# Kernel optimization log

Measured on AMD Instinct MI355X. Metric: run time of the kernel, lower is better.

## Reference

```python
import jax, jax.numpy as jnp
import numpy as np

N_IN = 100_000
N_OUT = 800_000
K = 27          # 3x3x3 kernel offsets
C_IN = 32
C_OUT = 64


def setup_inputs() -> dict:
    key = jax.random.key(0)
    k1, k2, k3, k4, k5, k6 = jax.random.split(key, 6)
    feats = jax.random.normal(k1, (N_IN, C_IN), dtype=jnp.float32)
    weight = jax.random.normal(k2, (K, C_IN, C_OUT), dtype=jnp.float32) * (1.0 / np.sqrt(C_IN * K))
    bias = jax.random.normal(k3, (C_OUT,), dtype=jnp.float32) * 0.01
    # bwd is the inverse sort permutation cached by the paired downsampling conv
    bwd = jax.random.permutation(k4, N_IN).astype(jnp.int64)
    # rulebook: per kernel offset, (input row, output row) pairs
    in_idx = jax.random.randint(k5, (K, N_IN), 0, N_IN, dtype=jnp.int64)
    out_idx = jax.random.randint(k6, (K, N_IN), 0, N_OUT, dtype=jnp.int64)
    return {"feats": feats, "weight": weight, "bias": bias,
            "bwd": bwd, "in_idx": in_idx, "out_idx": out_idx, "n_out": N_OUT}


def reference(feats, weight, bias, bwd, in_idx, out_idx, n_out):
    # 1) recover original feature order (the x.feats[bwd] gather)
    f = feats[bwd]                                   # [N_in, C_in]
    # 2) rulebook gather-GEMM-scatter
    gathered = f[in_idx]                             # [K, P, C_in]
    contrib = jnp.einsum('kpc,kcd->kpd', gathered, weight)  # [K, P, C_out]
    out = jnp.zeros((n_out, C_OUT), dtype=feats.dtype)
    out = out.at[out_idx].add(contrib)               # scatter-add over rulebook
    out = out + bias
    return out
```

## Files before the change

### kernel.cpp

```cpp
#include <hip/hip_runtime.h>

#define C_IN  32
#define C_OUT 64
#define KK    27

using frag_ab = __attribute__((ext_vector_type(8))) short;
using frag_cd = __attribute__((ext_vector_type(4))) float;
using u32x4   = __attribute__((ext_vector_type(4))) unsigned int;

static __device__ inline unsigned short f2bf(float f) {
    unsigned u = __float_as_uint(f);
    return (unsigned short)((u + 0x7fffu + ((u >> 16) & 1u)) >> 16);
}
static __device__ inline unsigned pack2(float a, float b) {
    return (unsigned)f2bf(a) | ((unsigned)f2bf(b) << 16);
}
static __device__ inline float bflo(unsigned u) { return __uint_as_float(u << 16); }
static __device__ inline float bfhi(unsigned u) { return __uint_as_float(u & 0xffff0000u); }

__global__ __launch_bounds__(256) void sic_init_bias(float4* __restrict__ out4,
                                                     const float4* __restrict__ bias4,
                                                     int total4) {
    int idx = blockIdx.x * 256 + threadIdx.x, stride = gridDim.x * 256;
    for (int i = idx; i < total4; i += stride) out4[i] = bias4[i & 15];
}

__global__ __launch_bounds__(256) void sic_scatter(
    const float* __restrict__ feats, const float* __restrict__ weight,
    const int* __restrict__ bwd, const int* __restrict__ in_idx,
    const int* __restrict__ out_idx, float* __restrict__ out, int n_in)
{
    const int k = blockIdx.y, lane = threadIdx.x & 63, wid = threadIdx.x >> 6;
    float w[C_IN];
    const float* wk = weight + k * (C_IN * C_OUT);
#pragma unroll
    for (int i = 0; i < C_IN; ++i) w[i] = wk[i * C_OUT + lane];
    const int waves_total = gridDim.x * 4;
    const long long base = (long long)k * n_in;
    for (int p = blockIdx.x * 4 + wid; p < n_in; p += waves_total) {
        int src = __builtin_amdgcn_readfirstlane(in_idx[base + p]);
        int dst = __builtin_amdgcn_readfirstlane(out_idx[base + p]);
        int row = __builtin_amdgcn_readfirstlane(bwd[src]);
        const float* f = feats + (long long)row * C_IN;
        float acc = 0.0f;
#pragma unroll
        for (int i = 0; i < C_IN; ++i) acc = fmaf(f[i], w[i], acc);
        atomicAdd(out + (long long)dst * C_OUT + lane, acc);
    }
}

__global__ __launch_bounds__(512) void sic_zero(int* __restrict__ p, int n) {
    int i = blockIdx.x * 512 + threadIdx.x, stride = gridDim.x * 512;
    for (; i < n; i += stride) p[i] = 0;
}

__global__ __launch_bounds__(256) void sic_fconv(const float* __restrict__ feats,
                                                 short* __restrict__ featsbf, int n_in) {
    int t = blockIdx.x * 256 + threadIdx.x;
    if (t >= (n_in + 1) * 4) return;
    int row = t >> 2, c8 = (t & 3) * 8;
    uint4 v = {0u, 0u, 0u, 0u};
    if (row < n_in) {
        const float* fp = feats + (size_t)row * C_IN + c8;
        float4 f0 = ((const float4*)fp)[0];
        float4 f1 = ((const float4*)fp)[1];
        v.x = pack2(f0.x, f0.y);
        v.y = pack2(f0.z, f0.w);
        v.z = pack2(f1.x, f1.y);
        v.w = pack2(f1.z, f1.w);
    }
    ((uint4*)featsbf)[t] = v;
}

__global__ __launch_bounds__(256) void sic_wconv(const float* __restrict__ weight,
                                                 short* __restrict__ wfrag) {
    int t = blockIdx.x * 256 + threadIdx.x;
    if (t >= KK * 4 * 64) return;
    int l = t & 63, nb = (t >> 6) & 3, k = t >> 8;
    int g = l >> 4, cl = l & 15;
    const float* wp = weight + (size_t)k * (C_IN * C_OUT) + nb * 16 + cl;
    float r[8];
#pragma unroll
    for (int j = 0; j < 8; ++j) r[j] = wp[(size_t)(g * 8 + j) * C_OUT];
    uint4 v = {pack2(r[0], r[1]), pack2(r[2], r[3]), pack2(r[4], r[5]), pack2(r[6], r[7])};
    ((uint4*)wfrag)[t] = v;
}

__global__ __launch_bounds__(256) void sic_hist3(const int* __restrict__ out_idx_seg,
                                                 int* __restrict__ count,
                                                 int* __restrict__ ord, int pseg) {
    int i = blockIdx.x * 256 + threadIdx.x;
    if (i < pseg) {
        ord[i] = atomicAdd(&count[out_idx_seg[i]], 1);
    }
}

__global__ __launch_bounds__(512) void sic_scan_chunk(const int* __restrict__ in,
                                                      int* __restrict__ outExcl,
                                                      int* __restrict__ sums, int n) {
    __shared__ int sm[512];
    int tid = threadIdx.x, g = blockIdx.x * 512 + tid;
    int e = (g < n) ? in[g] : 0;
    sm[tid] = e;
    __syncthreads();
    for (int off = 1; off < 512; off <<= 1) {
        int t = (tid >= off) ? sm[tid - off] : 0;
        __syncthreads();
        sm[tid] += t;
        __syncthreads();
    }
    if (g < n) outExcl[g] = sm[tid] - e;
    if (tid == 511) sums[blockIdx.x] = sm[511];
}

__global__ __launch_bounds__(512) void sic_scan_small(int* __restrict__ buf, int n) {
    __shared__ int sm[512];
    int tid = threadIdx.x;
    int e = (tid < n) ? buf[tid] : 0;
    sm[tid] = e;
    __syncthreads();
    for (int off = 1; off < 512; off <<= 1) {
        int t = (tid >= off) ? sm[tid - off] : 0;
        __syncthreads();
        sm[tid] += t;
        __syncthreads();
    }
    if (tid < n) buf[tid] = sm[tid] - e;
}

__global__ __launch_bounds__(512) void sic_scan_addback(int* __restrict__ arr,
                                                        const int* __restrict__ sums, int n) {
    int g = blockIdx.x * 512 + threadIdx.x;
    if (g < n) arr[g] += sums[blockIdx.x];
}

__global__ __launch_bounds__(256) void sic_gemm3(
    const int* __restrict__ in_idx,
    const int* __restrict__ out_idx,
    const int* __restrict__ bwd,
    const int* __restrict__ ord,
    const int* __restrict__ startv,
    const short* __restrict__ featsbf,
    const short* __restrict__ wfrag,
    unsigned short* __restrict__ contrib,
    int n_in, int k0, int zrow)
{
    __shared__ unsigned smU[4][16][40];
    const int kk   = k0 + blockIdx.y;
    const int lane = threadIdx.x & 63;
    const int wid  = threadIdx.x >> 6;
    const int g = lane >> 4, cl = lane & 15;

    const frag_ab wa0 = *(const frag_ab*)(wfrag + ((size_t)(kk * 4 + 0) * 64 + lane) * 8);
    const frag_ab wa1 = *(const frag_ab*)(wfrag + ((size_t)(kk * 4 + 1) * 64 + lane) * 8);
    const frag_ab wa2 = *(const frag_ab*)(wfrag + ((size_t)(kk * 4 + 2) * 64 + lane) * 8);
    const frag_ab wa3 = *(const frag_ab*)(wfrag + ((size_t)(kk * 4 + 3) * 64 + lane) * 8);
    const frag_cd zf = {0.f, 0.f, 0.f, 0.f};

    const size_t gk  = (size_t)kk * n_in;
    const size_t sk  = (size_t)blockIdx.y * n_in;
    const int t      = blockIdx.x * 4 + wid;
    const int tbase  = t * 16;
    const int idx    = tbase + cl;
    const bool valid = idx < n_in;

    int row = zrow, pos = 0;
    if (valid) {
        row = bwd[in_idx[gk + idx]];
        int dst = out_idx[gk + idx];
        pos = startv[dst] + ord[sk + idx];
    }

    frag_ab b = *(const frag_ab*)(featsbf + (size_t)row * C_IN + g * 8);
    frag_cd d0 = __builtin_amdgcn_mfma_f32_16x16x32_bf16(wa0, b, zf, 0, 0, 0);
    frag_cd d1 = __builtin_amdgcn_mfma_f32_16x16x32_bf16(wa1, b, zf, 0, 0, 0);
    frag_cd d2 = __builtin_amdgcn_mfma_f32_16x16x32_bf16(wa2, b, zf, 0, 0, 0);
    frag_cd d3 = __builtin_amdgcn_mfma_f32_16x16x32_bf16(wa3, b, zf, 0, 0, 0);

    smU[wid][cl][0  + g * 2 + 0] = pack2(d0[0], d0[1]);
    smU[wid][cl][0  + g * 2 + 1] = pack2(d0[2], d0[3]);
    smU[wid][cl][8  + g * 2 + 0] = pack2(d1[0], d1[1]);
    smU[wid][cl][8  + g * 2 + 1] = pack2(d1[2], d1[3]);
    smU[wid][cl][16 + g * 2 + 0] = pack2(d2[0], d2[1]);
    smU[wid][cl][16 + g * 2 + 1] = pack2(d2[2], d2[3]);
    smU[wid][cl][24 + g * 2 + 0] = pack2(d3[0], d3[1]);
    smU[wid][cl][24 + g * 2 + 1] = pack2(d3[2], d3[3]);
    __syncthreads();

#pragma unroll
    for (int p = 0; p < 2; ++p) {
        int r = (lane >> 3) + p * 8;
        int c = lane & 7;
        u32x4 v = {smU[wid][r][c * 4 + 0], smU[wid][r][c * 4 + 1],
                   smU[wid][r][c * 4 + 2], smU[wid][r][c * 4 + 3]};
        int pos_r = __shfl(pos, r, 64);
        if (tbase + r < n_in) {
            __builtin_nontemporal_store(v,
                (u32x4*)(contrib + (size_t)pos_r * C_OUT + c * 8));
        }
    }
}

__global__ __launch_bounds__(256) void sic_reduce4(
    const unsigned int* __restrict__ contribU,
    const int* __restrict__ startv, const int* __restrict__ count,
    const float* __restrict__ bias, float* __restrict__ out,
    int n_out, int first)
{
    int t = blockIdx.x * 256 + threadIdx.x;
    int dst = t >> 3, c8 = t & 7;
    if (dst >= n_out) return;
    int s = startv[dst], c = count[dst];

    size_t ob = (size_t)dst * C_OUT + c8 * 8;
    float4 a0, a1;
    if (first) {
        a0 = *(const float4*)(bias + c8 * 8);
        a1 = *(const float4*)(bias + c8 * 8 + 4);
    } else {
        a0 = *(const float4*)(out + ob);
        a1 = *(const float4*)(out + ob + 4);
    }
    const u32x4* p = (const u32x4*)(contribU + (size_t)s * 32) + c8;
    int j = 0;
    for (; j + 2 <= c; j += 2) {
        u32x4 va = __builtin_nontemporal_load(&p[(size_t)j * 8]);
        u32x4 vb = __builtin_nontemporal_load(&p[(size_t)(j + 1) * 8]);
        a0.x += bflo(va.x); a0.y += bfhi(va.x);
        a0.z += bflo(va.y); a0.w += bfhi(va.y);
        a1.x += bflo(va.z); a1.y += bfhi(va.z);
        a1.z += bflo(va.w); a1.w += bfhi(va.w);
        a0.x += bflo(vb.x); a0.y += bfhi(vb.x);
        a0.z += bflo(vb.y); a0.w += bfhi(vb.y);
        a1.x += bflo(vb.z); a1.y += bfhi(vb.z);
        a1.z += bflo(vb.w); a1.w += bfhi(vb.w);
    }
    if (j < c) {
        u32x4 va = __builtin_nontemporal_load(&p[(size_t)j * 8]);
        a0.x += bflo(va.x); a0.y += bfhi(va.x);
        a0.z += bflo(va.y); a0.w += bfhi(va.y);
        a1.x += bflo(va.z); a1.y += bfhi(va.z);
        a1.z += bflo(va.w); a1.w += bfhi(va.w);
    }
    *(float4*)(out + ob)     = a0;
    *(float4*)(out + ob + 4) = a1;
}

extern "C" void kernel_launch(void* const* d_in, const int* in_sizes, int n_in_cnt,
                              void* d_out, int out_size, void* d_ws, size_t ws_size,
                              hipStream_t stream) {
    const float* feats   = (const float*)d_in[0];
    const float* weight  = (const float*)d_in[1];
    const float* bias    = (const float*)d_in[2];
    const int*   bwd     = (const int*)d_in[3];
    const int*   in_idx  = (const int*)d_in[4];
    const int*   out_idx = (const int*)d_in[5];
    float*       out     = (float*)d_out;

    const int n_in  = in_sizes[0] / C_IN;
    const int n_out = out_size / C_OUT;
    const size_t P  = (size_t)KK * n_in;

    const int NCH1 = (n_out + 511) / 512;
    const int NCH2 = (NCH1 + 511) / 512;

    const size_t NOUTr   = ((size_t)n_out + 255) & ~(size_t)255;
    const size_t o_cnt   = 0;
    const size_t o_stv   = NOUTr;
    const size_t o_s1    = 2 * NOUTr;
    const size_t S1r     = ((size_t)NCH1 + 255) & ~(size_t)255;
    const size_t o_s1e   = o_s1 + S1r;
    const size_t o_s2    = o_s1e + S1r;
    const size_t o_ord   = (o_s2 + 512 + 255) & ~(size_t)255;
    const size_t o_fbf   = (o_ord + P + 255) & ~(size_t)255;
    const size_t fbf_i   = ((size_t)(n_in + 16) * C_IN * 2 + 3) / 4;
    const size_t o_wfr   = (o_fbf + fbf_i + 255) & ~(size_t)255;
    const size_t wfr_i   = (size_t)KK * 4 * 64 * 8 * 2 / 4;
    const size_t o_ctr   = (o_wfr + wfr_i + 255) & ~(size_t)255;

    const size_t ws_ints = ws_size / 4;
    size_t cap_recs = (ws_ints > o_ctr) ? (ws_ints - o_ctr) / 32 : 0;
    int kseg_max = (int)(cap_recs / (size_t)n_in);
    if (kseg_max > KK) kseg_max = KK;

    if (kseg_max < 1 || NCH2 > 512) {
        const int total4 = out_size / 4;
        hipLaunchKernelGGL(sic_init_bias, dim3(2048), dim3(256), 0, stream,
                           (float4*)out, (const float4*)bias, total4);
        hipLaunchKernelGGL(sic_scatter, dim3(160, KK), dim3(256), 0, stream,
                           feats, weight, bwd, in_idx, out_idx, out, n_in);
        return;
    }

    int* ws = (int*)d_ws;
    int* count  = ws + o_cnt;
    int* startv = ws + o_stv;
    int* sums1  = ws + o_s1;
    int* sums1e = ws + o_s1e;
    int* sums2  = ws + o_s2;
    int* ord    = ws + o_ord;
    short* featsbf = (short*)(ws + o_fbf);
    short* wfrag   = (short*)(ws + o_wfr);
    unsigned short* contrib = (unsigned short*)(ws + o_ctr);

    hipLaunchKernelGGL(sic_fconv, dim3(((n_in + 1) * 4 + 255) / 256), dim3(256), 0, stream,
                       feats, featsbf, n_in);
    hipLaunchKernelGGL(sic_wconv, dim3((KK * 4 * 64 + 255) / 256), dim3(256), 0, stream,
                       weight, wfrag);

    const int ntiles  = (n_in + 15) / 16;
    const int gx_gemm = (ntiles + 3) / 4;

    for (int k0 = 0; k0 < KK; k0 += kseg_max) {
        const int kseg = (KK - k0 < kseg_max) ? (KK - k0) : kseg_max;
        const int pseg = kseg * n_in;
        const int gp   = (pseg + 255) / 256;
        const int* oseg = out_idx + (size_t)k0 * n_in;

        hipLaunchKernelGGL(sic_zero, dim3(1024), dim3(512), 0, stream, count, n_out);
        hipLaunchKernelGGL(sic_hist3, dim3(gp), dim3(256), 0, stream,
                           oseg, count, ord, pseg);
        hipLaunchKernelGGL(sic_scan_chunk, dim3(NCH1), dim3(512), 0, stream,
                           count, startv, sums1, n_out);
        hipLaunchKernelGGL(sic_scan_chunk, dim3(NCH2), dim3(512), 0, stream,
                           sums1, sums1e, sums2, NCH1);
        hipLaunchKernelGGL(sic_scan_small, dim3(1), dim3(512), 0, stream, sums2, NCH2);
        hipLaunchKernelGGL(sic_scan_addback, dim3(NCH2), dim3(512), 0, stream,
                           sums1e, sums2, NCH1);
        hipLaunchKernelGGL(sic_scan_addback, dim3(NCH1), dim3(512), 0, stream,
                           startv, sums1e, n_out);
        hipLaunchKernelGGL(sic_gemm3, dim3(gx_gemm, kseg), dim3(256), 0, stream,
                           in_idx, out_idx, bwd, ord, startv,
                           featsbf, wfrag, contrib, n_in, k0, n_in);
        hipLaunchKernelGGL(sic_reduce4, dim3((n_out * 8 + 255) / 256), dim3(256), 0, stream,
                           (const unsigned int*)contrib, startv, count, bias, out,
                           n_out, (k0 == 0) ? 1 : 0);
    }
}
```

Before: 362.0 us.

## Write MFMA results directly in fragment order and simplify scan to two levels

The GEMM kernel drops its LDS staging transpose and barrier. Each lane now writes its packed bf16 MFMA outputs straight to the contribution buffer in the MFMA fragment channel order, and the reduce kernel remaps channels to match that permuted layout. The prefix scan over output counts handles four elements per thread, which cuts the five-kernel three-level scan to three launches. The direct stores are 32-byte per lane and no longer nontemporal, so write coalescing may change.

Result: slower. 393.3 us (+8.7%).

```diff
diff --git a/kernel.cpp b/kernel.cpp
--- a/kernel.cpp
+++ b/kernel.cpp
@@ -95,13 +95,18 @@
     }
 }
 
-__global__ __launch_bounds__(512) void sic_scan_chunk(const int* __restrict__ in,
-                                                      int* __restrict__ outExcl,
-                                                      int* __restrict__ sums, int n) {
+__global__ __launch_bounds__(512) void sic_scanA(const int* __restrict__ in,
+                                                 int* __restrict__ outExcl,
+                                                 int* __restrict__ sums, int n) {
     __shared__ int sm[512];
-    int tid = threadIdx.x, g = blockIdx.x * 512 + tid;
-    int e = (g < n) ? in[g] : 0;
-    sm[tid] = e;
+    int tid = threadIdx.x;
+    int base = blockIdx.x * 2048 + tid * 4;
+    int e0 = (base + 0 < n) ? in[base + 0] : 0;
+    int e1 = (base + 1 < n) ? in[base + 1] : 0;
+    int e2 = (base + 2 < n) ? in[base + 2] : 0;
+    int e3 = (base + 3 < n) ? in[base + 3] : 0;
+    int s = e0 + e1 + e2 + e3;
+    sm[tid] = s;
     __syncthreads();
     for (int off = 1; off < 512; off <<= 1) {
         int t = (tid >= off) ? sm[tid - off] : 0;
@@ -109,7 +114,11 @@
         sm[tid] += t;
         __syncthreads();
     }
-    if (g < n) outExcl[g] = sm[tid] - e;
+    int pre = sm[tid] - s;
+    if (base + 0 < n) outExcl[base + 0] = pre;
+    if (base + 1 < n) outExcl[base + 1] = pre + e0;
+    if (base + 2 < n) outExcl[base + 2] = pre + e0 + e1;
+    if (base + 3 < n) outExcl[base + 3] = pre + e0 + e1 + e2;
     if (tid == 511) sums[blockIdx.x] = sm[511];
 }
 
@@ -128,13 +137,16 @@
     if (tid < n) buf[tid] = sm[tid] - e;
 }
 
-__global__ __launch_bounds__(512) void sic_scan_addback(int* __restrict__ arr,
-                                                        const int* __restrict__ sums, int n) {
-    int g = blockIdx.x * 512 + threadIdx.x;
-    if (g < n) arr[g] += sums[blockIdx.x];
-}
-
-__global__ __launch_bounds__(256) void sic_gemm3(
+__global__ __launch_bounds__(512) void sic_addbackA(int* __restrict__ arr,
+                                                    const int* __restrict__ sums, int n) {
+    int s = sums[blockIdx.x];
+    int base = blockIdx.x * 2048 + threadIdx.x * 4;
+#pragma unroll
+    for (int i = 0; i < 4; ++i)
+        if (base + i < n) arr[base + i] += s;
+}
+
+__global__ __launch_bounds__(256) void sic_gemm4(
     const int* __restrict__ in_idx,
     const int* __restrict__ out_idx,
     const int* __restrict__ bwd,
@@ -142,10 +154,9 @@
     const int* __restrict__ startv,
     const short* __restrict__ featsbf,
     const short* __restrict__ wfrag,
-    unsigned short* __restrict__ contrib,
+    unsigned int* __restrict__ contribU,
     int n_in, int k0, int zrow)
 {
-    __shared__ unsigned smU[4][16][40];
     const int kk   = k0 + blockIdx.y;
     const int lane = threadIdx.x & 63;
     const int wid  = threadIdx.x >> 6;
@@ -160,8 +171,7 @@
     const size_t gk  = (size_t)kk * n_in;
     const size_t sk  = (size_t)blockIdx.y * n_in;
     const int t      = blockIdx.x * 4 + wid;
-    const int tbase  = t * 16;
-    const int idx    = tbase + cl;
+    const int idx    = t * 16 + cl;
     const bool valid = idx < n_in;
 
     int row = zrow, pos = 0;
@@ -177,31 +187,18 @@
     frag_cd d2 = __builtin_amdgcn_mfma_f32_16x16x32_bf16(wa2, b, zf, 0, 0, 0);
     frag_cd d3 = __builtin_amdgcn_mfma_f32_16x16x32_bf16(wa3, b, zf, 0, 0, 0);
 
-    smU[wid][cl][0  + g * 2 + 0] = pack2(d0[0], d0[1]);
-    smU[wid][cl][0  + g * 2 + 1] = pack2(d0[2], d0[3]);
-    smU[wid][cl][8  + g * 2 + 0] = pack2(d1[0], d1[1]);
-    smU[wid][cl][8  + g * 2 + 1] = pack2(d1[2], d1[3]);
-    smU[wid][cl][16 + g * 2 + 0] = pack2(d2[0], d2[1]);
-    smU[wid][cl][16 + g * 2 + 1] = pack2(d2[2], d2[3]);
-    smU[wid][cl][24 + g * 2 + 0] = pack2(d3[0], d3[1]);
-    smU[wid][cl][24 + g * 2 + 1] = pack2(d3[2], d3[3]);
-    __syncthreads();
-
-#pragma unroll
-    for (int p = 0; p < 2; ++p) {
-        int r = (lane >> 3) + p * 8;
-        int c = lane & 7;
-        u32x4 v = {smU[wid][r][c * 4 + 0], smU[wid][r][c * 4 + 1],
-                   smU[wid][r][c * 4 + 2], smU[wid][r][c * 4 + 3]};
-        int pos_r = __shfl(pos, r, 64);
-        if (tbase + r < n_in) {
-            __builtin_nontemporal_store(v,
-                (u32x4*)(contrib + (size_t)pos_r * C_OUT + c * 8));
-        }
-    }
-}
-
-__global__ __launch_bounds__(256) void sic_reduce4(
+    if (valid) {
+        unsigned int* cp = contribU + (size_t)pos * 32 + g * 8;
+        uint4 v0 = {pack2(d0[0], d0[1]), pack2(d0[2], d0[3]),
+                    pack2(d1[0], d1[1]), pack2(d1[2], d1[3])};
+        uint4 v1 = {pack2(d2[0], d2[1]), pack2(d2[2], d2[3]),
+                    pack2(d3[0], d3[1]), pack2(d3[2], d3[3])};
+        *(uint4*)(cp)     = v0;
+        *(uint4*)(cp + 4) = v1;
+    }
+}
+
+__global__ __launch_bounds__(256) void sic_reduce5(
     const unsigned int* __restrict__ contribU,
     const int* __restrict__ startv, const int* __restrict__ count,
     const float* __restrict__ bias, float* __restrict__ out,
@@ -212,14 +209,16 @@
     if (dst >= n_out) return;
     int s = startv[dst], c = count[dst];
 
-    size_t ob = (size_t)dst * C_OUT + c8 * 8;
+    const int chA = (c8 & 1) * 32 + (c8 >> 1) * 4;
+    size_t obA = (size_t)dst * C_OUT + chA;
+    size_t obB = obA + 16;
     float4 a0, a1;
     if (first) {
-        a0 = *(const float4*)(bias + c8 * 8);
-        a1 = *(const float4*)(bias + c8 * 8 + 4);
+        a0 = *(const float4*)(bias + chA);
+        a1 = *(const float4*)(bias + chA + 16);
     } else {
-        a0 = *(const float4*)(out + ob);
-        a1 = *(const float4*)(out + ob + 4);
+        a0 = *(const float4*)(out + obA);
+        a1 = *(const float4*)(out + obB);
     }
     const u32x4* p = (const u32x4*)(contribU + (size_t)s * 32) + c8;
     int j = 0;
@@ -242,8 +241,8 @@
         a1.x += bflo(va.z); a1.y += bfhi(va.z);
         a1.z += bflo(va.w); a1.w += bfhi(va.w);
     }
-    *(float4*)(out + ob)     = a0;
-    *(float4*)(out + ob + 4) = a1;
+    *(float4*)(out + obA) = a0;
+    *(float4*)(out + obB) = a1;
 }
 
 extern "C" void kernel_launch(void* const* d_in, const int* in_sizes, int n_in_cnt,
@@ -261,17 +260,13 @@
     const int n_out = out_size / C_OUT;
     const size_t P  = (size_t)KK * n_in;
 
-    const int NCH1 = (n_out + 511) / 512;
-    const int NCH2 = (NCH1 + 511) / 512;
+    const int NCHA = (n_out + 2047) / 2048;
 
     const size_t NOUTr   = ((size_t)n_out + 255) & ~(size_t)255;
     const size_t o_cnt   = 0;
     const size_t o_stv   = NOUTr;
     const size_t o_s1    = 2 * NOUTr;
-    const size_t S1r     = ((size_t)NCH1 + 255) & ~(size_t)255;
-    const size_t o_s1e   = o_s1 + S1r;
-    const size_t o_s2    = o_s1e + S1r;
-    const size_t o_ord   = (o_s2 + 512 + 255) & ~(size_t)255;
+    const size_t o_ord   = (o_s1 + 512 + 255) & ~(size_t)255;
     const size_t o_fbf   = (o_ord + P + 255) & ~(size_t)255;
     const size_t fbf_i   = ((size_t)(n_in + 16) * C_IN * 2 + 3) / 4;
     const size_t o_wfr   = (o_fbf + fbf_i + 255) & ~(size_t)255;
@@ -283,7 +278,7 @@
     int kseg_max = (int)(cap_recs / (size_t)n_in);
     if (kseg_max > KK) kseg_max = KK;
 
-    if (kseg_max < 1 || NCH2 > 512) {
+    if (kseg_max < 1 || NCHA > 512) {
         const int total4 = out_size / 4;
         hipLaunchKernelGGL(sic_init_bias, dim3(2048), dim3(256), 0, stream,
                            (float4*)out, (const float4*)bias, total4);
@@ -295,13 +290,11 @@
     int* ws = (int*)d_ws;
     int* count  = ws + o_cnt;
     int* startv = ws + o_stv;
-    int* sums1  = ws + o_s1;
-    int* sums1e = ws + o_s1e;
-    int* sums2  = ws + o_s2;
+    int* sums   = ws + o_s1;
     int* ord    = ws + o_ord;
     short* featsbf = (short*)(ws + o_fbf);
     short* wfrag   = (short*)(ws + o_wfr);
-    unsigned short* contrib = (unsigned short*)(ws + o_ctr);
+    unsigned int* contribU = (unsigned int*)(ws + o_ctr);
 
     hipLaunchKernelGGL(sic_fconv, dim3(((n_in + 1) * 4 + 255) / 256), dim3(256), 0, stream,
                        feats, featsbf, n_in);
@@ -320,20 +313,16 @@
         hipLaunchKernelGGL(sic_zero, dim3(1024), dim3(512), 0, stream, count, n_out);
         hipLaunchKernelGGL(sic_hist3, dim3(gp), dim3(256), 0, stream,
                            oseg, count, ord, pseg);
-        hipLaunchKernelGGL(sic_scan_chunk, dim3(NCH1), dim3(512), 0, stream,
-                           count, startv, sums1, n_out);
-        hipLaunchKernelGGL(sic_scan_chunk, dim3(NCH2), dim3(512), 0, stream,
-                           sums1, sums1e, sums2, NCH1);
-        hipLaunchKernelGGL(sic_scan_small, dim3(1), dim3(512), 0, stream, sums2, NCH2);
-        hipLaunchKernelGGL(sic_scan_addback, dim3(NCH2), dim3(512), 0, stream,
-                           sums1e, sums2, NCH1);
-        hipLaunchKernelGGL(sic_scan_addback, dim3(NCH1), dim3(512), 0, stream,
-                           startv, sums1e, n_out);
-        hipLaunchKernelGGL(sic_gemm3, dim3(gx_gemm, kseg), dim3(256), 0, stream,
+        hipLaunchKernelGGL(sic_scanA, dim3(NCHA), dim3(512), 0, stream,
+                           count, startv, sums, n_out);
+        hipLaunchKernelGGL(sic_scan_small, dim3(1), dim3(512), 0, stream, sums, NCHA);
+        hipLaunchKernelGGL(sic_addbackA, dim3(NCHA), dim3(512), 0, stream,
+                           startv, sums, n_out);
+        hipLaunchKernelGGL(sic_gemm4, dim3(gx_gemm, kseg), dim3(256), 0, stream,
                            in_idx, out_idx, bwd, ord, startv,
-                           featsbf, wfrag, contrib, n_in, k0, n_in);
-        hipLaunchKernelGGL(sic_reduce4, dim3((n_out * 8 + 255) / 256), dim3(256), 0, stream,
-                           (const unsigned int*)contrib, startv, count, bias, out,
+                           featsbf, wfrag, contribU, n_in, k0, n_in);
+        hipLaunchKernelGGL(sic_reduce5, dim3((n_out * 8 + 255) / 256), dim3(256), 0, stream,
+                           contribU, startv, count, bias, out,
                            n_out, (k0 == 0) ? 1 : 0);
     }
 }
```
